# Kernel tuning notes

Measured on AMD Instinct MI355X. Metric: run time of the kernel, lower is better.

## Reference

```python
import jax, jax.numpy as jnp
import numpy as np

B, S, HID = 2, 2048, 2048
NH, NKV, HD = 32, 8, 64
EPS = 1e-6
SCALE = HD ** -0.5


def rms_norm(x, w, eps=EPS):
    xf = x.astype(jnp.float32)
    var = jnp.mean(xf * xf, axis=-1, keepdims=True)
    return (w * (xf * jax.lax.rsqrt(var + eps))).astype(x.dtype)


def rotate_half(x):
    x1, x2 = jnp.split(x, 2, axis=-1)
    return jnp.concatenate((-x2, x1), axis=-1)


def setup_inputs() -> dict:
    key = jax.random.key(0)
    ks = jax.random.split(key, 8)
    hidden_states = jax.random.normal(ks[0], (B, S, HID), jnp.float32)
    # realistic RoPE tables
    inv_freq = 1.0 / (500000.0 ** (np.arange(0, HD, 2, dtype=np.float32) / HD))
    pos = np.arange(S, dtype=np.float32)
    freqs = np.outer(pos, inv_freq)                      # [S, HD/2]
    emb = np.concatenate([freqs, freqs], axis=-1)        # [S, HD]
    cos = jnp.broadcast_to(jnp.asarray(np.cos(emb)), (B, S, HD))
    sin = jnp.broadcast_to(jnp.asarray(np.sin(emb)), (B, S, HD))
    std = HID ** -0.5
    Wq = jax.random.normal(ks[1], (NH * HD, HID), jnp.float32) * std
    Wk = jax.random.normal(ks[2], (NKV * HD, HID), jnp.float32) * std
    Wv = jax.random.normal(ks[3], (NKV * HD, HID), jnp.float32) * std
    Wo = jax.random.normal(ks[4], (HID, NH * HD), jnp.float32) * std
    q_norm_w = jnp.ones((HD,), jnp.float32)
    k_norm_w = jnp.ones((HD,), jnp.float32)
    return {"hidden_states": hidden_states, "cos": cos, "sin": sin,
            "Wq": Wq, "Wk": Wk, "Wv": Wv, "Wo": Wo,
            "q_norm_w": q_norm_w, "k_norm_w": k_norm_w}


def reference(hidden_states, cos, sin, Wq, Wk, Wv, Wo, q_norm_w, k_norm_w):
    b, s, _ = hidden_states.shape
    # QKV projections (nn.Linear: x @ W.T)
    q = (hidden_states @ Wq.T).reshape(b, s, NH, HD).transpose(0, 2, 1, 3)   # [B,NH,S,D]
    k = (hidden_states @ Wk.T).reshape(b, s, NKV, HD).transpose(0, 2, 1, 3)  # [B,NKV,S,D]
    v = (hidden_states @ Wv.T).reshape(b, s, NKV, HD).transpose(0, 2, 1, 3)
    # per-head QK RMSNorm (use_head_qk_norm=True)
    q = rms_norm(q, q_norm_w)
    k = rms_norm(k, k_norm_w)
    # RoPE, cos/sin broadcast over heads (unsqueeze dim 1)
    c = cos[:, None, :, :]
    sn = sin[:, None, :, :]
    q = q * c + rotate_half(q) * sn
    k = k * c + rotate_half(k) * sn
    # GQA: expand kv heads to query heads
    groups = NH // NKV
    k = jnp.repeat(k, groups, axis=1)
    v = jnp.repeat(v, groups, axis=1)
    # eager SDPA, causal, softmax in fp32
    scores = jnp.einsum('bhqd,bhkd->bhqk', q, k) * SCALE
    causal = jnp.tril(jnp.ones((s, s), bool))
    scores = jnp.where(causal, scores, jnp.finfo(jnp.float32).min)
    probs = jax.nn.softmax(scores.astype(jnp.float32), axis=-1).astype(q.dtype)
    attn = jnp.einsum('bhqk,bhkd->bhqd', probs, v)       # [B,NH,S,D]
    attn = attn.transpose(0, 2, 1, 3).reshape(b, s, NH * HD)
    return attn @ Wo.T
```

## Files before the change

### kernel.cpp

```cpp
#include <hip/hip_runtime.h>
#include <hip/hip_bf16.h>
#include <stdint.h>

typedef __bf16 bf16;
typedef __bf16 bf16x8 __attribute__((ext_vector_type(8)));
typedef float floatx4 __attribute__((ext_vector_type(4)));
typedef float floatx8 __attribute__((ext_vector_type(8)));

#define MFMA16(A, B, C) __builtin_amdgcn_mfma_f32_16x16x32_bf16(A, B, C, 0, 0, 0)

constexpr int Sc = 2048, HIDc = 2048, NHc = 32, NKVc = 8, HDc = 64;
constexpr float kScale = 0.125f;
constexpr float kMax = 9.0f;

__device__ __forceinline__ void async16(const bf16* g, bf16* l) {
  __builtin_amdgcn_global_load_lds(
      (const __attribute__((address_space(1))) void*)g,
      (__attribute__((address_space(3))) void*)l, 16, 0, 0);
}

__global__ __launch_bounds__(256)
void cvt5(const float* __restrict__ s0, bf16* __restrict__ d0, int n0,
          const float* __restrict__ s1, bf16* __restrict__ d1, int n1,
          const float* __restrict__ s2, bf16* __restrict__ d2, int n2,
          const float* __restrict__ s3, bf16* __restrict__ d3, int n3,
          const float* __restrict__ s4, bf16* __restrict__ d4, int n4)
{
  const float* s; bf16* d; int n;
  switch (blockIdx.y) {
    case 0: s = s0; d = d0; n = n0; break;
    case 1: s = s1; d = d1; n = n1; break;
    case 2: s = s2; d = d2; n = n2; break;
    case 3: s = s3; d = d3; n = n3; break;
    default: s = s4; d = d4; n = n4; break;
  }
  const size_t stride = (size_t)gridDim.x * blockDim.x * 8;
  for (size_t i = ((size_t)blockIdx.x * blockDim.x + threadIdx.x) * 8;
       i < (size_t)n; i += stride) {
    floatx8 f = *(const floatx8*)(s + i);
    bf16x8 o;
#pragma unroll
    for (int j = 0; j < 8; ++j) o[j] = (bf16)f[j];
    *(bf16x8*)(d + i) = o;
  }
}

template<int BM, int BN, bool CF32>
__device__ __forceinline__
void gemm8p(const bf16* __restrict__ A, const bf16* __restrict__ Bw,
            void* __restrict__ C, int N, int K, int m0, int n0,
            bf16* __restrict__ lds)
{
  constexpr int MR2  = BM / 64;
  constexpr int ALD  = BM / 128;
  constexpr int BLD  = BN / 128;
  constexpr int AH   = BM * 32;
  constexpr int BH   = BN * 32;
  constexpr int GATE = ALD + BLD;

  const int tid  = threadIdx.x;
  const int lane = tid & 63;
  const int w    = tid >> 6;
  const int r    = lane & 15;
  const int quad = lane >> 4;
  const int wm   = w >> 2;
  const int wn   = w & 3;
  const int NT   = K >> 6;

  const bf16* gA[ALD]; const bf16* gB[BLD];
#pragma unroll
  for (int i = 0; i < ALD; ++i) {
    const int ch = i * 512 + tid;
    gA[i] = A + (size_t)(m0 + (ch >> 2)) * K + (ch & 3) * 8;
  }
#pragma unroll
  for (int i = 0; i < BLD; ++i) {
    const int ch = i * 512 + tid;
    gB[i] = Bw + (size_t)(n0 + (ch >> 2)) * K + (ch & 3) * 8;
  }

  auto stA = [&](int kt, int s, int kk) {
    bf16* dst = lds + (s * 2 + kk) * AH + tid * 8;
#pragma unroll
    for (int i = 0; i < ALD; ++i)
      async16(gA[i] + kt * 64 + kk * 32, dst + i * 4096);
  };
  auto stB = [&](int kt, int s, int kk) {
    bf16* dst = lds + 4 * AH + (s * 2 + kk) * BH + tid * 8;
#pragma unroll
    for (int i = 0; i < BLD; ++i)
      async16(gB[i] + kt * 64 + kk * 32, dst + i * 4096);
  };

  const int aoff = (wm * (BM / 2) + r) * 32 + quad * 8;
  const int boff = (wn * 64 + r) * 32 + quad * 8;

  floatx4 acc[2 * MR2][4] = {};
  bf16x8 a[MR2], b[4];

#define LDB(S, KK) do { const bf16* _p = lds + 4 * AH + ((S) * 2 + (KK)) * BH + boff; \
  _Pragma("unroll") for (int n2 = 0; n2 < 4; ++n2) b[n2] = *(const bf16x8*)(_p + n2 * 512); } while (0)
#define LDA(S, KK, MH) do { const bf16* _p = lds + ((S) * 2 + (KK)) * AH + aoff + (MH) * (MR2 * 512); \
  _Pragma("unroll") for (int m2 = 0; m2 < MR2; ++m2) a[m2] = *(const bf16x8*)(_p + m2 * 512); } while (0)
#define MM(MH) do { __builtin_amdgcn_s_setprio(1); \
  _Pragma("unroll") for (int m2 = 0; m2 < MR2; ++m2) \
    _Pragma("unroll") for (int n2 = 0; n2 < 4; ++n2) \
      acc[(MH) * MR2 + m2][n2] = MFMA16(a[m2], b[n2], acc[(MH) * MR2 + m2][n2]); \
  __builtin_amdgcn_s_setprio(0); } while (0)
#define BAR() asm volatile("s_barrier" ::: "memory")
#define GATEW() do { if constexpr (GATE == 4) asm volatile("s_waitcnt vmcnt(4)" ::: "memory"); \
                     else                     asm volatile("s_waitcnt vmcnt(3)" ::: "memory"); } while (0)

  stA(0, 0, 0); stB(0, 0, 0); stA(0, 0, 1); stB(0, 0, 1);
  stA(1, 1, 0); stB(1, 1, 0);
  GATEW(); BAR();

  for (int t = 0; t < NT; ++t) {
    const int s = t & 1;
    LDB(s, 0); LDA(s, 0, 0);
    if (t + 1 < NT) stA(t + 1, s ^ 1, 1);
    BAR(); MM(0); BAR();
    LDA(s, 0, 1);
    if (t + 1 < NT) stB(t + 1, s ^ 1, 1);
    BAR(); MM(1); BAR();
    LDB(s, 1); LDA(s, 1, 0);
    if (t + 2 < NT) stA(t + 2, s, 0);
    BAR(); MM(0); BAR();
    LDA(s, 1, 1);
    if (t + 2 < NT) stB(t + 2, s, 0);
    BAR(); MM(1);
    GATEW(); BAR();
  }

#undef LDB
#undef LDA
#undef MM
#undef BAR
#undef GATEW

#pragma unroll
  for (int mt = 0; mt < 2 * MR2; ++mt) {
#pragma unroll
    for (int nt = 0; nt < 4; ++nt) {
      const int row = m0 + wm * (BM / 2) + mt * 16 + quad * 4;
      const int col = n0 + wn * 64 + nt * 16 + r;
#pragma unroll
      for (int g = 0; g < 4; ++g) {
        const size_t ci = (size_t)(row + g) * N + col;
        const float v = acc[mt][nt][g];
        if constexpr (CF32) ((float*)C)[ci] = v;
        else                ((bf16*)C)[ci]  = (bf16)v;
      }
    }
  }
}

__global__ __launch_bounds__(512, 2)
void qkv_gemm8(const bf16* __restrict__ hs,
               const bf16* __restrict__ Wq, const bf16* __restrict__ Wk,
               const bf16* __restrict__ Wv,
               bf16* __restrict__ q_ws, bf16* __restrict__ k_ws,
               bf16* __restrict__ v_ws)
{
  __shared__ bf16 lds[2 * 2 * (256 + 256) * 32];
  const int wg  = blockIdx.x;
  const int swz = (wg & 7) * 24 + (wg >> 3);
  const int mi  = swz / 12, ni = swz % 12;
  const bf16* Bw; bf16* C; int N, n0;
  if (ni < 8)       { Bw = Wq; C = q_ws; N = 2048; n0 = ni * 256; }
  else if (ni < 10) { Bw = Wk; C = k_ws; N = 512;  n0 = (ni - 8) * 256; }
  else              { Bw = Wv; C = v_ws; N = 512;  n0 = (ni - 10) * 256; }
  gemm8p<256, 256, false>(hs, Bw, C, N, HIDc, mi * 256, n0, lds);
}

__global__ __launch_bounds__(512, 2)
void o_gemm8(const bf16* __restrict__ a_ws, const bf16* __restrict__ Wo,
             float* __restrict__ out)
{
  __shared__ bf16 lds[2 * 2 * (128 + 256) * 32];
  const int wg  = blockIdx.x;
  const int swz = (wg & 7) * 32 + (wg >> 3);
  const int mi  = swz >> 3, ni = swz & 7;
  gemm8p<128, 256, true>(a_ws, Wo, out, HIDc, NHc * HDc, mi * 128, ni * 256, lds);
}

__global__ __launch_bounds__(256)
void norm_rope_k(bf16* __restrict__ kk, const float* __restrict__ kw,
                 const float* __restrict__ cp, const float* __restrict__ sp)
{
  const int m = blockIdx.x;
  const int lane = threadIdx.x & 63;
  const int w = threadIdx.x >> 6;
  const float c  = cp[(size_t)m * 64 + lane];
  const float s  = sp[(size_t)m * 64 + lane];
  const float wk = kw[lane];
  for (int h = w; h < NKVc; h += 4) {
    bf16* p = kk + (size_t)m * (NKVc * HDc) + h * HDc + lane;
    float x = (float)*p;
    float ss = x * x;
#pragma unroll
    for (int off = 1; off < 64; off <<= 1) ss += __shfl_xor(ss, off);
    const float rr = rsqrtf(ss * (1.0f / 64.0f) + 1e-6f);
    const float y = wk * x * rr;
    const float partner = __shfl_xor(y, 32);
    const float rot = (lane < 32) ? -partner : partner;
    *p = (bf16)(y * c + rot * s);
  }
}

__global__ __launch_bounds__(256)
void v_transpose(const bf16* __restrict__ v, bf16* __restrict__ vt)
{
  __shared__ bf16 Ts[64 * 64];
  const int bi  = blockIdx.x;
  const int st  = bi & 31;
  const int kvh = (bi >> 5) & 7;
  const int b   = bi >> 8;
  const int tid = threadIdx.x;
  for (int seg = tid; seg < 512; seg += 256) {
    const int sr = seg >> 3, dc = (seg & 7) * 8;
    bf16x8 xv = *(const bf16x8*)(v + (size_t)(b * Sc + st * 64 + sr) * (NKVc * HDc)
                                   + kvh * HDc + dc);
#pragma unroll
    for (int i = 0; i < 8; ++i)
      Ts[(dc + i) * 64 + (sr ^ dc)] = xv[i];
  }
  __syncthreads();
  for (int seg = tid; seg < 512; seg += 256) {
    const int d = seg >> 3, sc = (seg & 7) * 8;
    bf16x8 yv = *(const bf16x8*)(&Ts[d * 64 + (sc ^ (d & 56))]);
    *(bf16x8*)(vt + ((size_t)((b * NKVc + kvh) * 64 + d)) * Sc + st * 64 + sc) = yv;
  }
}

__global__ __launch_bounds__(256, 4)
void attn_fwd(const bf16* __restrict__ q, const bf16* __restrict__ k,
              const bf16* __restrict__ vt, bf16* __restrict__ o,
              const float* __restrict__ qw, const float* __restrict__ cp,
              const float* __restrict__ sp)
{
  __shared__ bf16 Ks[64 * 64];
  __shared__ bf16 Vs[64 * 64];
  __shared__ bf16 Ps[4][16 * 72];

  const int bi  = blockIdx.x;
  const int pa  = bi & 15;
  const int h   = (bi >> 4) & 31;
  const int b   = bi >> 9;
  const int kvh = h >> 2;
  const int tid = threadIdx.x, lane = tid & 63, w = tid >> 6;
  const int r = lane & 15, quad = lane >> 4;
  const int qt0 = 31 - pa, qt1 = pa;

  const floatx8 w0 = *(const floatx8*)(qw + quad * 8);
  const floatx8 w1 = *(const floatx8*)(qw + 32 + quad * 8);
  bf16x8 qf[2][2];
#pragma unroll
  for (int t = 0; t < 2; ++t) {
    const int qt = t == 0 ? qt0 : qt1;
    const int m = b * Sc + qt * 64 + w * 16 + r;
    const bf16* qp = q + (size_t)m * (NHc * HDc) + h * HDc + quad * 8;
    bf16x8 x0 = *(const bf16x8*)qp;
    bf16x8 x1 = *(const bf16x8*)(qp + 32);
    float ss = 0.f;
#pragma unroll
    for (int i = 0; i < 8; ++i)
      ss += (float)x0[i] * (float)x0[i] + (float)x1[i] * (float)x1[i];
    ss += __shfl_xor(ss, 16);
    ss += __shfl_xor(ss, 32);
    const float rq = rsqrtf(ss * (1.0f / 64.0f) + 1e-6f) * kScale;
    const floatx8 c0 = *(const floatx8*)(cp + (size_t)m * 64 + quad * 8);
    const floatx8 c1 = *(const floatx8*)(cp + (size_t)m * 64 + 32 + quad * 8);
    const floatx8 s0 = *(const floatx8*)(sp + (size_t)m * 64 + quad * 8);
    const floatx8 s1 = *(const floatx8*)(sp + (size_t)m * 64 + 32 + quad * 8);
    bf16x8 y0v, y1v;
#pragma unroll
    for (int i = 0; i < 8; ++i) {
      const float y0 = (float)x0[i] * rq * w0[i];
      const float y1 = (float)x1[i] * rq * w1[i];
      y0v[i] = (bf16)(y0 * c0[i] - y1 * s0[i]);
      y1v[i] = (bf16)(y1 * c1[i] + y0 * s1[i]);
    }
    qf[t][0] = y0v; qf[t][1] = y1v;
  }

  floatx4 accO[2][4] = {};
  float lsum[2][4] = {};

  const int kvr = tid >> 3;
  const int cA  = (tid & 7) * 8;
  const int cx  = cA ^ (8 * (kvr & 7));
  const int xk  = 8 * (r & 15 & 7);

  const bf16* kp = k + (size_t)b * Sc * (NKVc * HDc) + kvh * HDc;
  const bf16* vp = vt + ((size_t)((b * NKVc + kvh) * 64)) * Sc;

  for (int j = 0; j <= qt0; ++j) {
    __syncthreads();
    {
      const bf16* kj = kp + (size_t)j * 64 * (NKVc * HDc);
      const bf16* vj = vp + j * 64;
      async16(kj + (size_t)kvr * (NKVc * HDc) + cx, Ks + tid * 8);
      async16(kj + (size_t)(kvr + 32) * (NKVc * HDc) + cx, Ks + (tid + 256) * 8);
      async16(vj + (size_t)kvr * Sc + cx, Vs + tid * 8);
      async16(vj + (size_t)(kvr + 32) * Sc + cx, Vs + (tid + 256) * 8);
    }
    __syncthreads();

#pragma unroll
    for (int t = 0; t < 2; ++t) {
      if (t == 1 && j > qt1) continue;
      const int qt = t == 0 ? qt0 : qt1;

      floatx4 sa[4];
#pragma unroll
      for (int nt = 0; nt < 4; ++nt) sa[nt] = floatx4{0.f, 0.f, 0.f, 0.f};
#pragma unroll
      for (int nt = 0; nt < 4; ++nt) {
        const int kv = nt * 16 + r;
        const bf16x8 kb0 = *(const bf16x8*)(&Ks[kv * 64 + ((quad * 8) ^ xk)]);
        const bf16x8 kb1 = *(const bf16x8*)(&Ks[kv * 64 + ((quad * 8 + 32) ^ xk)]);
        sa[nt] = MFMA16(qf[t][0], kb0, sa[nt]);
        sa[nt] = MFMA16(qf[t][1], kb1, sa[nt]);
      }

      const int maskbase = (j == qt) ? (w * 16 + quad * 4) : 1000;
#pragma unroll
      for (int reg = 0; reg < 4; ++reg) {
#pragma unroll
        for (int nt = 0; nt < 4; ++nt) {
          const float p = (nt * 16 + r <= maskbase + reg)
                              ? __expf(sa[nt][reg] - kMax) : 0.f;
          lsum[t][reg] += p;
          Ps[w][(quad * 4 + reg) * 72 + nt * 16 + r] = (bf16)p;
        }
      }

      const bf16x8 pa0 = *(const bf16x8*)(&Ps[w][r * 72 + quad * 8]);
      const bf16x8 pa1 = *(const bf16x8*)(&Ps[w][r * 72 + 32 + quad * 8]);
#pragma unroll
      for (int dt = 0; dt < 4; ++dt) {
        const int d = dt * 16 + r;
        const bf16x8 vb0 = *(const bf16x8*)(&Vs[d * 64 + ((quad * 8) ^ xk)]);
        const bf16x8 vb1 = *(const bf16x8*)(&Vs[d * 64 + ((quad * 8 + 32) ^ xk)]);
        accO[t][dt] = MFMA16(pa0, vb0, accO[t][dt]);
        accO[t][dt] = MFMA16(pa1, vb1, accO[t][dt]);
      }
    }
  }

#pragma unroll
  for (int t = 0; t < 2; ++t) {
    const int qt = t == 0 ? qt0 : qt1;
#pragma unroll
    for (int reg = 0; reg < 4; ++reg) {
      float l = lsum[t][reg];
#pragma unroll
      for (int off = 1; off < 16; off <<= 1) l += __shfl_xor(l, off);
      const float inv = 1.0f / l;
      const size_t row = (size_t)(b * Sc + qt * 64 + w * 16 + quad * 4 + reg);
#pragma unroll
      for (int dt = 0; dt < 4; ++dt)
        o[row * (NHc * HDc) + h * HDc + dt * 16 + r] = (bf16)(accO[t][dt][reg] * inv);
    }
  }
}

extern "C" void kernel_launch(void* const* d_in, const int* in_sizes, int n_in,
                              void* d_out, int out_size, void* d_ws, size_t ws_size,
                              hipStream_t stream)
{
  const float* hs = (const float*)d_in[0];
  const float* cp = (const float*)d_in[1];
  const float* sp = (const float*)d_in[2];
  const float* Wq = (const float*)d_in[3];
  const float* Wk = (const float*)d_in[4];
  const float* Wv = (const float*)d_in[5];
  const float* Wo = (const float*)d_in[6];
  const float* qw = (const float*)d_in[7];
  const float* kw = (const float*)d_in[8];
  float* out = (float*)d_out;

  char* ws = (char*)d_ws;
  bf16* q_ws  = (bf16*)ws;
  bf16* k_ws  = (bf16*)(ws + (16u << 20));
  bf16* v_ws  = (bf16*)(ws + (20u << 20));
  bf16* vt_ws = (bf16*)(ws + (24u << 20));
  bf16* hs_b  = (bf16*)(ws + (28u << 20));
  bf16* Wq_b  = (bf16*)(ws + (44u << 20));
  bf16* Wk_b  = (bf16*)(ws + (52u << 20));
  bf16* Wv_b  = (bf16*)(ws + (54u << 20));
  bf16* Wo_b  = (bf16*)(ws + (56u << 20));
  bf16* a_ws  = q_ws;

  dim3 blk(256);
  cvt5<<<dim3(256, 5), blk, 0, stream>>>(
      hs, hs_b, 4096 * 2048, Wq, Wq_b, 2048 * 2048, Wk, Wk_b, 512 * 2048,
      Wv, Wv_b, 512 * 2048, Wo, Wo_b, 2048 * 2048);
  qkv_gemm8<<<dim3(192), dim3(512), 0, stream>>>(hs_b, Wq_b, Wk_b, Wv_b,
                                                 q_ws, k_ws, v_ws);
  norm_rope_k<<<dim3(4096), blk, 0, stream>>>(k_ws, kw, cp, sp);
  v_transpose<<<dim3(512), blk, 0, stream>>>(v_ws, vt_ws);
  attn_fwd<<<dim3(1024), blk, 0, stream>>>(q_ws, k_ws, vt_ws, a_ws, qw, cp, sp);
  o_gemm8<<<dim3(256), dim3(512), 0, stream>>>(a_ws, Wo_b, out);
}
```

Measured before the change: 302.2 us.

## Fuse K norm/RoPE and V transpose into QKV GEMM epilogue; double-buffer attention K/V

Moves the per-head RMSNorm plus RoPE for K, and the V transpose, into the QKV GEMM epilogue. This removes two separate kernel launches and their workspace round trips. The attention kernel double-buffers K/V tiles in LDS, prefetching the next tile while computing the current one. It also splits the causal-mask path from the unmasked path and adds MFMA priority hints. Occupancy is lowered to 3 blocks because LDS use grows, and the fused epilogue writes strided V stores.

```diff
diff --git a/kernel.cpp b/kernel.cpp
--- a/kernel.cpp
+++ b/kernel.cpp
@@ -3,6 +3,7 @@
 #include <stdint.h>
 
 typedef __bf16 bf16;
+typedef __bf16 bf16x4 __attribute__((ext_vector_type(4)));
 typedef __bf16 bf16x8 __attribute__((ext_vector_type(8)));
 typedef float floatx4 __attribute__((ext_vector_type(4)));
 typedef float floatx8 __attribute__((ext_vector_type(8)));
@@ -45,11 +46,11 @@
   }
 }
 
-template<int BM, int BN, bool CF32>
+template<int BM, int BN>
 __device__ __forceinline__
-void gemm8p(const bf16* __restrict__ A, const bf16* __restrict__ Bw,
-            void* __restrict__ C, int N, int K, int m0, int n0,
-            bf16* __restrict__ lds)
+void gemm8p_core(const bf16* __restrict__ A, const bf16* __restrict__ Bw,
+                 int K, int m0, int n0, bf16* __restrict__ lds,
+                 floatx4 (&acc)[BM / 32][4])
 {
   constexpr int MR2  = BM / 64;
   constexpr int ALD  = BM / 128;
@@ -95,7 +96,6 @@
   const int aoff = (wm * (BM / 2) + r) * 32 + quad * 8;
   const int boff = (wn * 64 + r) * 32 + quad * 8;
 
-  floatx4 acc[2 * MR2][4] = {};
   bf16x8 a[MR2], b[4];
 
 #define LDB(S, KK) do { const bf16* _p = lds + 4 * AH + ((S) * 2 + (KK)) * BH + boff; \
@@ -137,20 +137,78 @@
 #undef MM
 #undef BAR
 #undef GATEW
-
-#pragma unroll
-  for (int mt = 0; mt < 2 * MR2; ++mt) {
+}
+
+template<int MT, bool CF32>
+__device__ __forceinline__
+void epi_plain(const floatx4 (&acc)[MT][4], void* C, int N, int m0, int n0,
+               int BMh, int wm, int wn, int r, int quad)
+{
+#pragma unroll
+  for (int mt = 0; mt < MT; ++mt) {
 #pragma unroll
     for (int nt = 0; nt < 4; ++nt) {
-      const int row = m0 + wm * (BM / 2) + mt * 16 + quad * 4;
+      const int row = m0 + wm * BMh + mt * 16 + quad * 4;
       const int col = n0 + wn * 64 + nt * 16 + r;
 #pragma unroll
       for (int g = 0; g < 4; ++g) {
         const size_t ci = (size_t)(row + g) * N + col;
-        const float v = acc[mt][nt][g];
-        if constexpr (CF32) ((float*)C)[ci] = v;
-        else                ((bf16*)C)[ci]  = (bf16)v;
+        if constexpr (CF32) ((float*)C)[ci] = acc[mt][nt][g];
+        else                ((bf16*)C)[ci]  = (bf16)acc[mt][nt][g];
       }
+    }
+  }
+}
+
+template<int MT>
+__device__ __forceinline__
+void epi_k(const floatx4 (&acc)[MT][4], bf16* kws, const float* kw,
+           const float* cp, const float* sp, int m0, int n0,
+           int wm, int wn, int r, int quad)
+{
+  const int h = (n0 >> 6) + wn;
+  const float w0 = kw[r], w1 = kw[16 + r], w2 = kw[32 + r], w3 = kw[48 + r];
+#pragma unroll
+  for (int mt = 0; mt < MT; ++mt) {
+#pragma unroll
+    for (int g = 0; g < 4; ++g) {
+      const int row = m0 + wm * 128 + mt * 16 + quad * 4 + g;
+      const float x0 = acc[mt][0][g], x1 = acc[mt][1][g];
+      const float x2 = acc[mt][2][g], x3 = acc[mt][3][g];
+      float ss = x0 * x0 + x1 * x1 + x2 * x2 + x3 * x3;
+      ss += __shfl_xor(ss, 1); ss += __shfl_xor(ss, 2);
+      ss += __shfl_xor(ss, 4); ss += __shfl_xor(ss, 8);
+      const float rr = rsqrtf(ss * (1.0f / 64.0f) + 1e-6f);
+      const float y0 = x0 * rr * w0, y1 = x1 * rr * w1;
+      const float y2 = x2 * rr * w2, y3 = x3 * rr * w3;
+      const float* cb = cp + (size_t)row * 64 + r;
+      const float* sb = sp + (size_t)row * 64 + r;
+      bf16* p = kws + (size_t)row * 512 + h * 64 + r;
+      p[0]  = (bf16)(y0 * cb[0]  - y2 * sb[0]);
+      p[16] = (bf16)(y1 * cb[16] - y3 * sb[16]);
+      p[32] = (bf16)(y2 * cb[32] + y0 * sb[32]);
+      p[48] = (bf16)(y3 * cb[48] + y1 * sb[48]);
+    }
+  }
+}
+
+template<int MT>
+__device__ __forceinline__
+void epi_v(const floatx4 (&acc)[MT][4], bf16* vt, int m0, int n0,
+           int wm, int wn, int r, int quad)
+{
+  const int kvh = (n0 >> 6) + wn;
+  const int b   = m0 >> 11;
+  const int sb  = (m0 & 2047) + wm * 128 + quad * 4;
+#pragma unroll
+  for (int mt = 0; mt < MT; ++mt) {
+#pragma unroll
+    for (int nt = 0; nt < 4; ++nt) {
+      const int d = nt * 16 + r;
+      bf16x4 pk;
+#pragma unroll
+      for (int g = 0; g < 4; ++g) pk[g] = (bf16)acc[mt][nt][g];
+      *(bf16x4*)(vt + ((size_t)((b * 8 + kvh) * 64 + d)) * Sc + sb + mt * 16) = pk;
     }
   }
 }
@@ -160,17 +218,31 @@
                const bf16* __restrict__ Wq, const bf16* __restrict__ Wk,
                const bf16* __restrict__ Wv,
                bf16* __restrict__ q_ws, bf16* __restrict__ k_ws,
-               bf16* __restrict__ v_ws)
+               bf16* __restrict__ vt_ws,
+               const float* __restrict__ kw, const float* __restrict__ cp,
+               const float* __restrict__ sp)
 {
   __shared__ bf16 lds[2 * 2 * (256 + 256) * 32];
   const int wg  = blockIdx.x;
   const int swz = (wg & 7) * 24 + (wg >> 3);
   const int mi  = swz / 12, ni = swz % 12;
-  const bf16* Bw; bf16* C; int N, n0;
-  if (ni < 8)       { Bw = Wq; C = q_ws; N = 2048; n0 = ni * 256; }
-  else if (ni < 10) { Bw = Wk; C = k_ws; N = 512;  n0 = (ni - 8) * 256; }
-  else              { Bw = Wv; C = v_ws; N = 512;  n0 = (ni - 10) * 256; }
-  gemm8p<256, 256, false>(hs, Bw, C, N, HIDc, mi * 256, n0, lds);
+  const bf16* Bw; int n0;
+  if (ni < 8)       { Bw = Wq; n0 = ni * 256; }
+  else if (ni < 10) { Bw = Wk; n0 = (ni - 8) * 256; }
+  else              { Bw = Wv; n0 = (ni - 10) * 256; }
+
+  floatx4 acc[8][4] = {};
+  gemm8p_core<256, 256>(hs, Bw, HIDc, mi * 256, n0, lds, acc);
+
+  const int lane = threadIdx.x & 63, w = threadIdx.x >> 6;
+  const int r = lane & 15, quad = lane >> 4;
+  const int wm = w >> 2, wn = w & 3;
+  if (ni < 8)
+    epi_plain<8, false>(acc, q_ws, 2048, mi * 256, n0, 128, wm, wn, r, quad);
+  else if (ni < 10)
+    epi_k<8>(acc, k_ws, kw, cp, sp, mi * 256, n0, wm, wn, r, quad);
+  else
+    epi_v<8>(acc, vt_ws, mi * 256, n0, wm, wn, r, quad);
 }
 
 __global__ __launch_bounds__(512, 2)
@@ -181,66 +253,24 @@
   const int wg  = blockIdx.x;
   const int swz = (wg & 7) * 32 + (wg >> 3);
   const int mi  = swz >> 3, ni = swz & 7;
-  gemm8p<128, 256, true>(a_ws, Wo, out, HIDc, NHc * HDc, mi * 128, ni * 256, lds);
-}
-
-__global__ __launch_bounds__(256)
-void norm_rope_k(bf16* __restrict__ kk, const float* __restrict__ kw,
-                 const float* __restrict__ cp, const float* __restrict__ sp)
-{
-  const int m = blockIdx.x;
-  const int lane = threadIdx.x & 63;
-  const int w = threadIdx.x >> 6;
-  const float c  = cp[(size_t)m * 64 + lane];
-  const float s  = sp[(size_t)m * 64 + lane];
-  const float wk = kw[lane];
-  for (int h = w; h < NKVc; h += 4) {
-    bf16* p = kk + (size_t)m * (NKVc * HDc) + h * HDc + lane;
-    float x = (float)*p;
-    float ss = x * x;
-#pragma unroll
-    for (int off = 1; off < 64; off <<= 1) ss += __shfl_xor(ss, off);
-    const float rr = rsqrtf(ss * (1.0f / 64.0f) + 1e-6f);
-    const float y = wk * x * rr;
-    const float partner = __shfl_xor(y, 32);
-    const float rot = (lane < 32) ? -partner : partner;
-    *p = (bf16)(y * c + rot * s);
-  }
-}
-
-__global__ __launch_bounds__(256)
-void v_transpose(const bf16* __restrict__ v, bf16* __restrict__ vt)
-{
-  __shared__ bf16 Ts[64 * 64];
-  const int bi  = blockIdx.x;
-  const int st  = bi & 31;
-  const int kvh = (bi >> 5) & 7;
-  const int b   = bi >> 8;
-  const int tid = threadIdx.x;
-  for (int seg = tid; seg < 512; seg += 256) {
-    const int sr = seg >> 3, dc = (seg & 7) * 8;
-    bf16x8 xv = *(const bf16x8*)(v + (size_t)(b * Sc + st * 64 + sr) * (NKVc * HDc)
-                                   + kvh * HDc + dc);
-#pragma unroll
-    for (int i = 0; i < 8; ++i)
-      Ts[(dc + i) * 64 + (sr ^ dc)] = xv[i];
-  }
-  __syncthreads();
-  for (int seg = tid; seg < 512; seg += 256) {
-    const int d = seg >> 3, sc = (seg & 7) * 8;
-    bf16x8 yv = *(const bf16x8*)(&Ts[d * 64 + (sc ^ (d & 56))]);
-    *(bf16x8*)(vt + ((size_t)((b * NKVc + kvh) * 64 + d)) * Sc + st * 64 + sc) = yv;
-  }
-}
-
-__global__ __launch_bounds__(256, 4)
+
+  floatx4 acc[4][4] = {};
+  gemm8p_core<128, 256>(a_ws, Wo, NHc * HDc, mi * 128, ni * 256, lds, acc);
+
+  const int lane = threadIdx.x & 63, w = threadIdx.x >> 6;
+  const int r = lane & 15, quad = lane >> 4;
+  const int wm = w >> 2, wn = w & 3;
+  epi_plain<4, true>(acc, out, HIDc, mi * 128, ni * 256, 64, wm, wn, r, quad);
+}
+
+__global__ __launch_bounds__(256, 3)
 void attn_fwd(const bf16* __restrict__ q, const bf16* __restrict__ k,
               const bf16* __restrict__ vt, bf16* __restrict__ o,
               const float* __restrict__ qw, const float* __restrict__ cp,
               const float* __restrict__ sp)
 {
-  __shared__ bf16 Ks[64 * 64];
-  __shared__ bf16 Vs[64 * 64];
+  __shared__ bf16 Ks[2 * 64 * 64];
+  __shared__ bf16 Vs[2 * 64 * 64];
   __shared__ bf16 Ps[4][16 * 72];
 
   const int bi  = blockIdx.x;
@@ -251,6 +281,25 @@
   const int tid = threadIdx.x, lane = tid & 63, w = tid >> 6;
   const int r = lane & 15, quad = lane >> 4;
   const int qt0 = 31 - pa, qt1 = pa;
+
+  const int kvr = tid >> 3;
+  const int cx  = ((tid & 7) * 8) ^ (8 * (kvr & 7));
+  const int xk  = 8 * (r & 7);
+
+  const bf16* kp = k + (size_t)b * Sc * (NKVc * HDc) + kvh * HDc;
+  const bf16* vp = vt + ((size_t)((b * NKVc + kvh) * 64)) * Sc;
+
+  auto stage = [&](int j, int sb) {
+    const bf16* kj = kp + (size_t)j * 64 * (NKVc * HDc);
+    const bf16* vj = vp + j * 64;
+    bf16* Kd = Ks + sb * 4096;
+    bf16* Vd = Vs + sb * 4096;
+    async16(kj + (size_t)kvr * (NKVc * HDc) + cx, Kd + tid * 8);
+    async16(kj + (size_t)(kvr + 32) * (NKVc * HDc) + cx, Kd + (tid + 256) * 8);
+    async16(vj + (size_t)kvr * Sc + cx, Vd + tid * 8);
+    async16(vj + (size_t)(kvr + 32) * Sc + cx, Vd + (tid + 256) * 8);
+  };
+  stage(0, 0);
 
   const floatx8 w0 = *(const floatx8*)(qw + quad * 8);
   const floatx8 w1 = *(const floatx8*)(qw + 32 + quad * 8);
@@ -287,25 +336,12 @@
   floatx4 accO[2][4] = {};
   float lsum[2][4] = {};
 
-  const int kvr = tid >> 3;
-  const int cA  = (tid & 7) * 8;
-  const int cx  = cA ^ (8 * (kvr & 7));
-  const int xk  = 8 * (r & 15 & 7);
-
-  const bf16* kp = k + (size_t)b * Sc * (NKVc * HDc) + kvh * HDc;
-  const bf16* vp = vt + ((size_t)((b * NKVc + kvh) * 64)) * Sc;
-
   for (int j = 0; j <= qt0; ++j) {
+    const int sb = j & 1;
     __syncthreads();
-    {
-      const bf16* kj = kp + (size_t)j * 64 * (NKVc * HDc);
-      const bf16* vj = vp + j * 64;
-      async16(kj + (size_t)kvr * (NKVc * HDc) + cx, Ks + tid * 8);
-      async16(kj + (size_t)(kvr + 32) * (NKVc * HDc) + cx, Ks + (tid + 256) * 8);
-      async16(vj + (size_t)kvr * Sc + cx, Vs + tid * 8);
-      async16(vj + (size_t)(kvr + 32) * Sc + cx, Vs + (tid + 256) * 8);
-    }
-    __syncthreads();
+    if (j < qt0) stage(j + 1, sb ^ 1);
+    const bf16* Kb = Ks + sb * 4096;
+    const bf16* Vb = Vs + sb * 4096;
 
 #pragma unroll
     for (int t = 0; t < 2; ++t) {
@@ -315,37 +351,51 @@
       floatx4 sa[4];
 #pragma unroll
       for (int nt = 0; nt < 4; ++nt) sa[nt] = floatx4{0.f, 0.f, 0.f, 0.f};
+      __builtin_amdgcn_s_setprio(1);
 #pragma unroll
       for (int nt = 0; nt < 4; ++nt) {
         const int kv = nt * 16 + r;
-        const bf16x8 kb0 = *(const bf16x8*)(&Ks[kv * 64 + ((quad * 8) ^ xk)]);
-        const bf16x8 kb1 = *(const bf16x8*)(&Ks[kv * 64 + ((quad * 8 + 32) ^ xk)]);
+        const bf16x8 kb0 = *(const bf16x8*)(&Kb[kv * 64 + ((quad * 8) ^ xk)]);
+        const bf16x8 kb1 = *(const bf16x8*)(&Kb[kv * 64 + ((quad * 8 + 32) ^ xk)]);
         sa[nt] = MFMA16(qf[t][0], kb0, sa[nt]);
         sa[nt] = MFMA16(qf[t][1], kb1, sa[nt]);
       }
-
-      const int maskbase = (j == qt) ? (w * 16 + quad * 4) : 1000;
-#pragma unroll
-      for (int reg = 0; reg < 4; ++reg) {
-#pragma unroll
-        for (int nt = 0; nt < 4; ++nt) {
-          const float p = (nt * 16 + r <= maskbase + reg)
-                              ? __expf(sa[nt][reg] - kMax) : 0.f;
-          lsum[t][reg] += p;
-          Ps[w][(quad * 4 + reg) * 72 + nt * 16 + r] = (bf16)p;
-        }
+      __builtin_amdgcn_s_setprio(0);
+
+      if (j != qt) {
+#pragma unroll
+        for (int g = 0; g < 4; ++g)
+#pragma unroll
+          for (int nt = 0; nt < 4; ++nt) {
+            const float p = __expf(sa[nt][g] - kMax);
+            lsum[t][g] += p;
+            Ps[w][(quad * 4 + g) * 72 + nt * 16 + r] = (bf16)p;
+          }
+      } else {
+        const int maskbase = w * 16 + quad * 4;
+#pragma unroll
+        for (int g = 0; g < 4; ++g)
+#pragma unroll
+          for (int nt = 0; nt < 4; ++nt) {
+            const float p = (nt * 16 + r <= maskbase + g)
+                                ? __expf(sa[nt][g] - kMax) : 0.f;
+            lsum[t][g] += p;
+            Ps[w][(quad * 4 + g) * 72 + nt * 16 + r] = (bf16)p;
+          }
       }
 
       const bf16x8 pa0 = *(const bf16x8*)(&Ps[w][r * 72 + quad * 8]);
       const bf16x8 pa1 = *(const bf16x8*)(&Ps[w][r * 72 + 32 + quad * 8]);
+      __builtin_amdgcn_s_setprio(1);
 #pragma unroll
       for (int dt = 0; dt < 4; ++dt) {
         const int d = dt * 16 + r;
-        const bf16x8 vb0 = *(const bf16x8*)(&Vs[d * 64 + ((quad * 8) ^ xk)]);
-        const bf16x8 vb1 = *(const bf16x8*)(&Vs[d * 64 + ((quad * 8 + 32) ^ xk)]);
+        const bf16x8 vb0 = *(const bf16x8*)(&Vb[d * 64 + ((quad * 8) ^ xk)]);
+        const bf16x8 vb1 = *(const bf16x8*)(&Vb[d * 64 + ((quad * 8 + 32) ^ xk)]);
         accO[t][dt] = MFMA16(pa0, vb0, accO[t][dt]);
         accO[t][dt] = MFMA16(pa1, vb1, accO[t][dt]);
       }
+      __builtin_amdgcn_s_setprio(0);
     }
   }
 
@@ -376,6 +426,7 @@
   const float* Wq = (const float*)d_in[3];
   const float* Wk = (const float*)d_in[4];
   const float* Wv = (const float*)d_in[5];
+  const float* Wv_unused = Wv; (void)Wv_unused;
   const float* Wo = (const float*)d_in[6];
   const float* qw = (const float*)d_in[7];
   const float* kw = (const float*)d_in[8];
@@ -384,7 +435,6 @@
   char* ws = (char*)d_ws;
   bf16* q_ws  = (bf16*)ws;
   bf16* k_ws  = (bf16*)(ws + (16u << 20));
-  bf16* v_ws  = (bf16*)(ws + (20u << 20));
   bf16* vt_ws = (bf16*)(ws + (24u << 20));
   bf16* hs_b  = (bf16*)(ws + (28u << 20));
   bf16* Wq_b  = (bf16*)(ws + (44u << 20));
@@ -398,9 +448,7 @@
       hs, hs_b, 4096 * 2048, Wq, Wq_b, 2048 * 2048, Wk, Wk_b, 512 * 2048,
       Wv, Wv_b, 512 * 2048, Wo, Wo_b, 2048 * 2048);
   qkv_gemm8<<<dim3(192), dim3(512), 0, stream>>>(hs_b, Wq_b, Wk_b, Wv_b,
-                                                 q_ws, k_ws, v_ws);
-  norm_rope_k<<<dim3(4096), blk, 0, stream>>>(k_ws, kw, cp, sp);
-  v_transpose<<<dim3(512), blk, 0, stream>>>(v_ws, vt_ws);
+                                                 q_ws, k_ws, vt_ws, kw, cp, sp);
   attn_fwd<<<dim3(1024), blk, 0, stream>>>(q_ws, k_ws, vt_ws, a_ws, qw, cp, sp);
   o_gemm8<<<dim3(256), dim3(512), 0, stream>>>(a_ws, Wo_b, out);
 }
```

Result: slower. 316.1 us (+4.6%).
